# Optimization experiments

Hardware: AMD Instinct MI355X
Metric: run time of the kernel (lower is better)

The kernel has to match this reference:

```python
import jax, jax.numpy as jnp
import numpy as np

EMBED_DIM = 1024
N_HEADS = 16
HEAD_DIM = EMBED_DIM // N_HEADS
B, S = 2, 2048


def setup_inputs() -> dict:
    key = jax.random.key(0)
    ks = jax.random.split(key, 7)
    scale = 1.0 / np.sqrt(EMBED_DIM)
    return {
        "query": jax.random.normal(ks[0], (B, S, EMBED_DIM), dtype=jnp.float32),
        "key": jax.random.normal(ks[1], (B, S, EMBED_DIM), dtype=jnp.float32),
        "value": jax.random.normal(ks[2], (B, S, EMBED_DIM), dtype=jnp.float32),
        # nn.Linear weights stored as [out, in]; y = x @ W.T
        "Wq": jax.random.normal(ks[3], (EMBED_DIM, EMBED_DIM), dtype=jnp.float32) * scale,
        "Wk": jax.random.normal(ks[4], (EMBED_DIM, EMBED_DIM), dtype=jnp.float32) * scale,
        "Wv": jax.random.normal(ks[5], (EMBED_DIM, EMBED_DIM), dtype=jnp.float32) * scale,
        "Wo": jax.random.normal(ks[6], (EMBED_DIM, EMBED_DIM), dtype=jnp.float32) * scale,
    }


def reference(query, key, value, Wq, Wk, Wv, Wo):
    # Projections (Linear, no bias): x @ W.T
    Q = query @ Wq.T  # [B, S, E]
    K = key @ Wk.T
    V = value @ Wv.T
    b, s, _ = Q.shape
    # Split heads: slicing head i of [..., E] == reshape to [B, S, H, D]
    Qh = Q.reshape(b, s, N_HEADS, HEAD_DIM)
    Kh = K.reshape(b, s, N_HEADS, HEAD_DIM)
    Vh = V.reshape(b, s, N_HEADS, HEAD_DIM)
    scores = jnp.einsum("bqhd,bkhd->bhqk", Qh, Kh) / jnp.sqrt(
        jnp.asarray(HEAD_DIM, dtype=Qh.dtype)
    )  # [B, H, Sq, Sk]
    attn = jax.nn.softmax(scores, axis=-1)
    out = jnp.einsum("bhqk,bkhd->bqhd", attn, Vh)  # [B, Sq, H, D]
    out = out.reshape(b, s, N_HEADS * HEAD_DIM)  # concat heads
    return out @ Wo.T
```

## Files before the change

### kernel.cpp

```cpp
#include <hip/hip_runtime.h>
#include <hip/hip_bf16.h>
#include <stdint.h>
#include <stddef.h>

#define EMBED 1024
#define NHEAD 16
#define HDIM  64
#define BATCH 2
#define SEQ   2048
#define MTOT  (BATCH*SEQ)

typedef __hip_bfloat16 bf16;
typedef __attribute__((ext_vector_type(8))) __bf16 bf16x8;
typedef __attribute__((ext_vector_type(4))) float  f32x4;
typedef __attribute__((ext_vector_type(16))) float f32x16;

#define GLD16(gp, lp) __builtin_amdgcn_global_load_lds( \
    (__attribute__((address_space(1))) void*)(gp),      \
    (__attribute__((address_space(3))) void*)(lp), 16, 0, 0)


__device__ __forceinline__ ushort4 cvt4(const float4 v) {
  union { ushort4 u; bf16 b[4]; } o;
  o.b[0] = __float2bfloat16(v.x);
  o.b[1] = __float2bfloat16(v.y);
  o.b[2] = __float2bfloat16(v.z);
  o.b[3] = __float2bfloat16(v.w);
  return o.u;
}

__device__ __forceinline__ uint32_t pk2(float lo, float hi) {
  union { bf16 h[2]; uint32_t u; } r;
  r.h[0] = __float2bfloat16(lo);
  r.h[1] = __float2bfloat16(hi);
  return r.u;
}

__device__ __forceinline__ bool detect_bf16(const uint32_t* __restrict__ x, int t) {
  uint32_t w = x[(size_t)(t & 63) * 997u];
  int e = (int)((w >> 7) & 0xFF);
  unsigned long long m = __ballot(e >= 100 && e <= 135);
  return __popcll(m) >= 48;
}

#define SM_C1 0.18033688011112042f
#define SM_C0 -14.426950408889634f

__global__ __launch_bounds__(256)
void convert_inputs(const void* xs0, const void* xs1, const void* xs2,
                    const void* ws0, const void* ws1, const void* ws2, const void* ws3,
                    bf16* __restrict__ xd0, bf16* __restrict__ xd1, bf16* __restrict__ xd2,
                    bf16* __restrict__ wd0, bf16* __restrict__ wd1,
                    bf16* __restrict__ wd2, bf16* __restrict__ wd3) {
  const int bid = blockIdx.x;
  const void* src; bf16* dst; size_t base;
  if (bid < 6144) {
    const int a = bid >> 11;
    src = a == 0 ? xs0 : a == 1 ? xs1 : xs2;
    dst = a == 0 ? xd0 : a == 1 ? xd1 : xd2;
    base = (size_t)(bid & 2047) * 2048;
  } else {
    const int a = (bid - 6144) >> 9;
    src = a == 0 ? ws0 : a == 1 ? ws1 : a == 2 ? ws2 : ws3;
    dst = a == 0 ? wd0 : a == 1 ? wd1 : a == 2 ? wd2 : wd3;
    base = (size_t)((bid - 6144) & 511) * 2048;
  }
  const bool isbf = detect_bf16((const uint32_t*)src, threadIdx.x);
  const size_t off = base + (size_t)threadIdx.x * 8;
  if (isbf) {
    *(uint4*)((ushort*)dst + off) = *(const uint4*)((const ushort*)src + off);
  } else {
    const float* s = (const float*)src + off;
    float4 a4 = *(const float4*)(s);
    float4 b4 = *(const float4*)(s + 4);
    *(ushort4*)((ushort*)dst + off)     = cvt4(a4);
    *(ushort4*)((ushort*)dst + off + 4) = cvt4(b4);
  }
}

template<int TM, int TN>
__device__ __forceinline__ void gemm_nt_dbuf(
    const bf16* __restrict__ X, const bf16* __restrict__ W,
    bf16* sA, bf16* sB, f32x4 (&acc)[TM/32][TN/32],
    int row0, int col0, int t, int wr, int wc, int l16, int quad,
    int k0, int klen) {
  constexpr int CA = TM / 32, CB = TN / 32;
  constexpr int RI = TM / 32, RJ = TN / 32;
  constexpr int PF  = CA + CB;
  const int nit = klen >> 6;

  const bf16* gA[CA]; const bf16* gB[CB];
  int la[CA], lb[CB];
#pragma unroll
  for (int c = 0; c < CA; ++c) {
    int id = c * 256 + t, r = id >> 3;
    int cc = (((id & 7) ^ (r & 7)) * 8);
    gA[c] = X + (size_t)(row0 + r) * EMBED + k0 + cc;  la[c] = id * 8;
  }
#pragma unroll
  for (int c = 0; c < CB; ++c) {
    int id = c * 256 + t, r = id >> 3;
    int cc = (((id & 7) ^ (r & 7)) * 8);
    gB[c] = W + (size_t)(col0 + r) * EMBED + k0 + cc;  lb[c] = id * 8;
  }

  auto issue = [&](int kb, int buf) {
#pragma unroll
    for (int c = 0; c < CA; ++c) GLD16(gA[c] + kb, sA + buf * (TM * 64) + la[c]);
#pragma unroll
    for (int c = 0; c < CB; ++c) GLD16(gB[c] + kb, sB + buf * (TN * 64) + lb[c]);
  };
  const int xr = l16 & 7;
  auto compute = [&](int buf) {
    const bf16* pA = sA + buf * (TM * 64);
    const bf16* pB = sB + buf * (TN * 64);
#pragma unroll
    for (int kk = 0; kk < 64; kk += 32) {
      const int ch = (kk >> 3) + quad;
      bf16x8 a[RI], b[RJ];
#pragma unroll
      for (int i = 0; i < RI; ++i)
        a[i] = *(const bf16x8*)(pA + (wr + 16 * i + l16) * 64 + ((ch ^ xr) << 3));
#pragma unroll
      for (int j = 0; j < RJ; ++j)
        b[j] = *(const bf16x8*)(pB + (wc + 16 * j + l16) * 64 + ((ch ^ xr) << 3));
#pragma unroll
      for (int i = 0; i < RI; ++i)
#pragma unroll
        for (int j = 0; j < RJ; ++j)
          acc[i][j] = __builtin_amdgcn_mfma_f32_16x16x32_bf16(a[i], b[j], acc[i][j], 0, 0, 0);
    }
  };

  issue(0, 0);
  int p = 0;
  for (int i = 0; i < nit - 1; ++i) {
    issue((i + 1) * 64, p ^ 1);
    asm volatile("s_waitcnt vmcnt(%0)\ns_barrier" :: "i"(PF) : "memory");
    compute(p);
    asm volatile("s_barrier" ::: "memory");
    p ^= 1;
  }
  asm volatile("s_waitcnt vmcnt(0)\ns_barrier" ::: "memory");
  compute(p);
}

template<int TM, int TN, bool ABF, bool BBF>
__device__ __forceinline__ void gemm_nt_slow(
    const void* __restrict__ X, const void* __restrict__ W,
    bf16* sA, bf16* sB, f32x4 (&acc)[TM/32][TN/32],
    int row0, int col0, int t, int wr, int wc, int l16, int quad,
    int k0, int klen) {
  constexpr int RI = TM / 32, RJ = TN / 32;
  const int xr = l16 & 7;
  for (int kb = k0; kb < k0 + klen; kb += 64) {
    if constexpr (ABF) {
      const bf16* s = (const bf16*)X;
#pragma unroll
      for (int c = 0; c < TM / 32; ++c) {
        int id = c * 256 + t, r = id >> 3;
        int cc = (((id & 7) ^ (r & 7)) * 8);
        GLD16(s + (size_t)(row0 + r) * EMBED + kb + cc, sA + id * 8);
      }
    } else {
      const float* s = (const float*)X;
#pragma unroll
      for (int c = 0; c < TM / 16; ++c) {
        int id = c * 256 + t, r = id >> 4;
        int lc = (id & 15) >> 1, half = (id & 1) * 4;
        float4 v = *(const float4*)(s + (size_t)(row0 + r) * EMBED + kb + lc * 8 + half);
        *(ushort4*)(sA + r * 64 + ((lc ^ (r & 7)) << 3) + half) = cvt4(v);
      }
    }
    if constexpr (BBF) {
      const bf16* s = (const bf16*)W;
#pragma unroll
      for (int c = 0; c < TN / 32; ++c) {
        int id = c * 256 + t, r = id >> 3;
        int cc = (((id & 7) ^ (r & 7)) * 8);
        GLD16(s + (size_t)(col0 + r) * EMBED + kb + cc, sB + id * 8);
      }
    } else {
      const float* s = (const float*)W;
#pragma unroll
      for (int c = 0; c < TN / 16; ++c) {
        int id = c * 256 + t, r = id >> 4;
        int lc = (id & 15) >> 1, half = (id & 1) * 4;
        float4 v = *(const float4*)(s + (size_t)(col0 + r) * EMBED + kb + lc * 8 + half);
        *(ushort4*)(sB + r * 64 + ((lc ^ (r & 7)) << 3) + half) = cvt4(v);
      }
    }
    __syncthreads();
#pragma unroll
    for (int kk = 0; kk < 64; kk += 32) {
      const int ch = (kk >> 3) + quad;
      bf16x8 a[RI], b[RJ];
#pragma unroll
      for (int i = 0; i < RI; ++i)
        a[i] = *(const bf16x8*)(sA + (wr + 16 * i + l16) * 64 + ((ch ^ xr) << 3));
#pragma unroll
      for (int j = 0; j < RJ; ++j)
        b[j] = *(const bf16x8*)(sB + (wc + 16 * j + l16) * 64 + ((ch ^ xr) << 3));
#pragma unroll
      for (int i = 0; i < RI; ++i)
#pragma unroll
        for (int j = 0; j < RJ; ++j)
          acc[i][j] = __builtin_amdgcn_mfma_f32_16x16x32_bf16(a[i], b[j], acc[i][j], 0, 0, 0);
    }
    __syncthreads();
  }
}

__global__ __launch_bounds__(256, 2)
void qkv_proj_kernel(const void* Xq, const void* Xk, const void* Xv,
                     const void* Wq, const void* Wk, const void* Wv,
                     bf16* __restrict__ Qo, bf16* __restrict__ Ko,
                     bf16* __restrict__ Vto) {
  __shared__ __align__(16) bf16 sA[2 * 128 * 64];
  __shared__ __align__(16) bf16 sB[2 * 128 * 64];
  const int t    = threadIdx.x;
  const int wave = t >> 6, lane = t & 63;
  const int quad = lane >> 4, l16 = lane & 15;
  const int wr = (wave & 1) * 64;
  const int wc = (wave >> 1) * 64;
  const bool isbf = detect_bf16((const uint32_t*)Xq, t);

  for (int ti = blockIdx.x; ti < 768; ti += 512) {
    const int sel  = ti >> 8;
    const int col0 = ((ti >> 5) & 7) * 128;
    const int row0 = (ti & 31) * 128;
    const void* X = (sel == 0) ? Xq : (sel == 1) ? Xk : Xv;
    const void* W = (sel == 0) ? Wq : (sel == 1) ? Wk : Wv;

    f32x4 acc[4][4] = {};
    if (isbf)
      gemm_nt_dbuf<128, 128>((const bf16*)X, (const bf16*)W, sA, sB, acc,
                             row0, col0, t, wr, wc, l16, quad, 0, EMBED);
    else
      gemm_nt_slow<128, 128, false, false>(X, W, sA, sB, acc,
                                           row0, col0, t, wr, wc, l16, quad, 0, EMBED);

    if (sel < 2) {
      bf16* C = (sel == 0) ? Qo : Ko;
      const float sc = (sel == 0) ? SM_C1 : 1.0f;
#pragma unroll
      for (int i = 0; i < 4; ++i)
#pragma unroll
        for (int j = 0; j < 4; ++j)
#pragma unroll
          for (int r = 0; r < 4; ++r) {
            int m = row0 + wr + 16 * i + quad * 4 + r;
            int n = col0 + wc + 16 * j + l16;
            C[(size_t)m * EMBED + n] = __float2bfloat16(acc[i][j][r] * sc);
          }
    } else {
#pragma unroll
      for (int i = 0; i < 4; ++i)
#pragma unroll
        for (int j = 0; j < 4; ++j)
#pragma unroll
          for (int r = 0; r < 4; ++r) {
            int m = row0 + wr + 16 * i + quad * 4 + r;
            int n = col0 + wc + 16 * j + l16;
            int b = m >> 11, s = m & (SEQ - 1);
            int h = n >> 6,  d = n & (HDIM - 1);
            Vto[(((size_t)(b * NHEAD + h)) * HDIM + d) * SEQ + s] =
                __float2bfloat16(acc[i][j][r]);
          }
    }
    __syncthreads();
  }
}

__global__ __launch_bounds__(256, 2)
void out_proj_partial(const bf16* __restrict__ X, const void* W,
                      const uint32_t* __restrict__ qref, float* __restrict__ P) {
  __shared__ __align__(16) bf16 sA[2 * 128 * 64];
  __shared__ __align__(16) bf16 sB[2 * 128 * 64];
  const int t    = threadIdx.x;
  const int wave = t >> 6, lane = t & 63;
  const int quad = lane >> 4, l16 = lane & 15;
  const int row0 = blockIdx.x * 128;
  const int col0 = blockIdx.y * 128;
  const int z    = blockIdx.z;
  const int wr = (wave & 1) * 64;
  const int wc = (wave >> 1) * 64;
  const bool isbf = detect_bf16(qref, t);

  f32x4 acc[4][4] = {};
  if (isbf)
    gemm_nt_dbuf<128, 128>(X, (const bf16*)W, sA, sB, acc,
                           row0, col0, t, wr, wc, l16, quad, z * 512, 512);
  else
    gemm_nt_slow<128, 128, true, false>(X, W, sA, sB, acc,
                                        row0, col0, t, wr, wc, l16, quad, z * 512, 512);

  float* Pz = P + (size_t)z * MTOT * EMBED;
#pragma unroll
  for (int i = 0; i < 4; ++i)
#pragma unroll
    for (int j = 0; j < 4; ++j)
#pragma unroll
      for (int r = 0; r < 4; ++r) {
        int m = row0 + wr + 16 * i + quad * 4 + r;
        int n = col0 + wc + 16 * j + l16;
        Pz[(size_t)m * EMBED + n] = acc[i][j][r];
      }
}

__global__ __launch_bounds__(256)
void reduce_splitk(const float* __restrict__ P,
                   const uint32_t* __restrict__ qref, void* __restrict__ C) {
  const bool isbf = detect_bf16(qref, threadIdx.x);
  size_t i = ((size_t)blockIdx.x * 256 + threadIdx.x) * 4;
  float4 a = *(const float4*)(P + i);
  float4 b = *(const float4*)(P + (size_t)MTOT * EMBED + i);
  float4 s = make_float4(a.x + b.x, a.y + b.y, a.z + b.z, a.w + b.w);
  if (isbf) *(ushort4*)((bf16*)C + i) = cvt4(s);
  else      *(float4*)((float*)C + i) = s;
}

__global__ __launch_bounds__(256, 2)
void out_proj_kernel(const bf16* __restrict__ X, const void* W,
                     const uint32_t* __restrict__ qref, void* C) {
  __shared__ __align__(16) bf16 sA[2 * 64 * 64];
  __shared__ __align__(16) bf16 sB[2 * 128 * 64];
  const int t    = threadIdx.x;
  const int wave = t >> 6, lane = t & 63;
  const int quad = lane >> 4, l16 = lane & 15;
  const int row0 = blockIdx.x * 64;
  const int col0 = blockIdx.y * 128;
  const int wr = (wave & 1) * 32;
  const int wc = (wave >> 1) * 64;
  const bool isbf = detect_bf16(qref, t);

  f32x4 acc[2][4] = {};
  if (isbf)
    gemm_nt_dbuf<64, 128>(X, (const bf16*)W, sA, sB, acc,
                          row0, col0, t, wr, wc, l16, quad, 0, EMBED);
  else
    gemm_nt_slow<64, 128, true, false>(X, W, sA, sB, acc,
                                       row0, col0, t, wr, wc, l16, quad, 0, EMBED);

#pragma unroll
  for (int i = 0; i < 2; ++i)
#pragma unroll
    for (int j = 0; j < 4; ++j)
#pragma unroll
      for (int r = 0; r < 4; ++r) {
        int m = row0 + wr + 16 * i + quad * 4 + r;
        int n = col0 + wc + 16 * j + l16;
        if (isbf)
          ((bf16*)C)[(size_t)m * EMBED + n] = __float2bfloat16(acc[i][j][r]);
        else
          ((float*)C)[(size_t)m * EMBED + n] = acc[i][j][r];
      }
}

__global__ __launch_bounds__(256, 2)
void flash_kernel(const bf16* __restrict__ Q, const bf16* __restrict__ K,
                  const bf16* __restrict__ Vt, bf16* __restrict__ O) {
  __shared__ __align__(16) bf16 sK[2][64 * 64];
  __shared__ __align__(16) bf16 sV[2][64 * 64];

  const int t    = threadIdx.x;
  const int wave = t >> 6, lane = t & 63;
  const int l5 = lane & 31, hi = lane >> 5;
  const int x5 = l5 & 7;

  const int L  = ((blockIdx.x & 7) << 6) + (blockIdx.x >> 3);
  const int qt = L & 15;
  const int h  = (L >> 4) & 15;
  const int b  = L >> 8;
  const int qw = qt * 128 + 32 * wave;

  const bf16* Kg = K + ((size_t)b * SEQ) * EMBED + h * HDIM;
  const bf16* Vg = Vt + (((size_t)(b * NHEAD + h)) * HDIM) * SEQ;

  bf16x8 aq[4];
  {
    const bf16* Qrow = Q + ((size_t)b * SEQ + qw + l5) * EMBED + h * HDIM + hi * 8;
#pragma unroll
    for (int g = 0; g < 4; ++g) aq[g] = *(const bf16x8*)(Qrow + 16 * g);
  }

  union { bf16x8 v; bf16 e[8]; } ones;
#pragma unroll
  for (int i = 0; i < 8; ++i) ones.e[i] = __float2bfloat16(1.0f);

  auto issueKV = [&](int kt, int buf) {
#pragma unroll
    for (int c = 0; c < 2; ++c) {
      int id = c * 256 + t, r = id >> 3;
      int cc = (((id & 7) ^ (r & 7)) * 8);
      GLD16(Kg + (size_t)(kt + r) * EMBED + cc, &sK[buf][id * 8]);
      GLD16(Vg + (size_t)r * SEQ + kt + cc,     &sV[buf][id * 8]);
    }
  };

  f32x16 o0 = {}, o1 = {};
  f32x16 ls = {};

  auto tile_compute = [&](int buf) {
    f32x16 sT0, sT1;
#pragma unroll
    for (int r = 0; r < 16; ++r) { sT0[r] = SM_C0; sT1[r] = SM_C0; }
#pragma unroll
    for (int g = 0; g < 4; ++g) {
      const int ch = 2 * g + hi;
      bf16x8 ak0 = *(const bf16x8*)(&sK[buf][(l5)      * 64 + ((ch ^ x5) << 3)]);
      bf16x8 ak1 = *(const bf16x8*)(&sK[buf][(32 + l5) * 64 + ((ch ^ x5) << 3)]);
      sT0 = __builtin_amdgcn_mfma_f32_32x32x16_bf16(ak0, aq[g], sT0, 0, 0, 0);
      sT1 = __builtin_amdgcn_mfma_f32_32x32x16_bf16(ak1, aq[g], sT1, 0, 0, 0);
    }

    bf16x8 PA[4];
#pragma unroll
    for (int kg = 0; kg < 2; ++kg) {
      float p[16];
#pragma unroll
      for (int r = 0; r < 16; ++r)
        p[r] = __builtin_amdgcn_exp2f(kg ? sT1[r] : sT0[r]);
#pragma unroll
      for (int s = 0; s < 2; ++s) {
        uint32_t c0 = pk2(p[8 * s + 0], p[8 * s + 1]);
        uint32_t c1 = pk2(p[8 * s + 2], p[8 * s + 3]);
        uint32_t c2 = pk2(p[8 * s + 4], p[8 * s + 5]);
        uint32_t c3 = pk2(p[8 * s + 6], p[8 * s + 7]);
        uint32_t x = __shfl_xor(hi ? c0 : c2, 32, 64);
        uint32_t y = __shfl_xor(hi ? c1 : c3, 32, 64);
        union { uint32_t u[4]; bf16x8 v; } w;
        w.u[0] = hi ? x  : c0;
        w.u[1] = hi ? y  : c1;
        w.u[2] = hi ? c2 : x;
        w.u[3] = hi ? c3 : y;
        PA[2 * kg + s] = w.v;
      }
    }

#pragma unroll
    for (int kk = 0; kk < 4; ++kk) {
      const int ch = 2 * kk + hi;
      ls = __builtin_amdgcn_mfma_f32_32x32x16_bf16(PA[kk], ones.v, ls, 0, 0, 0);
      bf16x8 bv0 = *(const bf16x8*)(&sV[buf][(l5)      * 64 + ((ch ^ x5) << 3)]);
      bf16x8 bv1 = *(const bf16x8*)(&sV[buf][(32 + l5) * 64 + ((ch ^ x5) << 3)]);
      o0 = __builtin_amdgcn_mfma_f32_32x32x16_bf16(PA[kk], bv0, o0, 0, 0, 0);
      o1 = __builtin_amdgcn_mfma_f32_32x32x16_bf16(PA[kk], bv1, o1, 0, 0, 0);
    }
  };

  issueKV(0, 0);
  int p = 0;
  for (int it = 0; it < SEQ / 64 - 1; ++it) {
    issueKV((it + 1) * 64, p ^ 1);
    asm volatile("s_waitcnt vmcnt(4)\ns_barrier" ::: "memory");
    tile_compute(p);
    asm volatile("s_barrier" ::: "memory");
    p ^= 1;
  }
  asm volatile("s_waitcnt vmcnt(0)\ns_barrier" ::: "memory");
  tile_compute(p);

  bf16* Og = O + ((size_t)b * SEQ + qw) * EMBED + h * HDIM + l5;
#pragma unroll
  for (int r = 0; r < 16; ++r) {
    const int m = (r & 3) + 8 * (r >> 2) + 4 * hi;
    const float inv = 1.0f / ls[r];
    Og[(size_t)m * EMBED]      = __float2bfloat16(o0[r] * inv);
    Og[(size_t)m * EMBED + 32] = __float2bfloat16(o1[r] * inv);
  }
}

extern "C" void kernel_launch(void* const* d_in, const int* in_sizes, int n_in,
                              void* d_out, int out_size, void* d_ws, size_t ws_size,
                              hipStream_t stream) {
  (void)in_sizes; (void)n_in; (void)out_size;
  bf16* Qp  = (bf16*)((char*)d_ws + 256);
  bf16* Kp  = Qp  + (size_t)MTOT * EMBED;
  bf16* Vtp = Kp  + (size_t)MTOT * EMBED;
  bf16* Op  = Vtp + (size_t)MTOT * EMBED;
  float* Pf = (float*)(Op + (size_t)MTOT * EMBED);

  bf16* Xqb = (bf16*)Pf;
  bf16* Xkb = Xqb + (size_t)MTOT * EMBED;
  bf16* Xvb = Xkb + (size_t)MTOT * EMBED;
  bf16* Wqb = Xvb + (size_t)MTOT * EMBED;
  bf16* Wkb = Wqb + (size_t)EMBED * EMBED;
  bf16* Wvb = Wkb + (size_t)EMBED * EMBED;
  bf16* Wob = (bf16*)((char*)Pf + (size_t)2 * MTOT * EMBED * 4);

  const size_t need_split = 256 + (size_t)MTOT * EMBED * 2 * 4
                          + (size_t)MTOT * EMBED * 4 * 2;
  const size_t need_conv  = need_split + (size_t)EMBED * EMBED * 2;

  if (ws_size >= need_conv) {
    convert_inputs<<<dim3(8192), 256, 0, stream>>>(
        d_in[0], d_in[1], d_in[2], d_in[3], d_in[4], d_in[5], d_in[6],
        Xqb, Xkb, Xvb, Wqb, Wkb, Wvb, Wob);
    qkv_proj_kernel<<<dim3(512), 256, 0, stream>>>(
        Xqb, Xkb, Xvb, Wqb, Wkb, Wvb, Qp, Kp, Vtp);
    flash_kernel<<<dim3(512), 256, 0, stream>>>(Qp, Kp, Vtp, Op);
    out_proj_partial<<<dim3(32, 8, 2), 256, 0, stream>>>(
        Op, Wob, (const uint32_t*)Qp, Pf);
    reduce_splitk<<<dim3(MTOT * EMBED / 1024), 256, 0, stream>>>(
        Pf, (const uint32_t*)d_in[0], d_out);
  } else if (ws_size >= need_split) {
    qkv_proj_kernel<<<dim3(512), 256, 0, stream>>>(
        d_in[0], d_in[1], d_in[2], d_in[3], d_in[4], d_in[5], Qp, Kp, Vtp);
    flash_kernel<<<dim3(512), 256, 0, stream>>>(Qp, Kp, Vtp, Op);
    out_proj_partial<<<dim3(32, 8, 2), 256, 0, stream>>>(
        Op, d_in[6], (const uint32_t*)d_in[0], Pf);
    reduce_splitk<<<dim3(MTOT * EMBED / 1024), 256, 0, stream>>>(
        Pf, (const uint32_t*)d_in[0], d_out);
  } else {
    qkv_proj_kernel<<<dim3(512), 256, 0, stream>>>(
        d_in[0], d_in[1], d_in[2], d_in[3], d_in[4], d_in[5], Qp, Kp, Vtp);
    flash_kernel<<<dim3(512), 256, 0, stream>>>(Qp, Kp, Vtp, Op);
    out_proj_kernel<<<dim3(64, 8), 256, 0, stream>>>(
        Op, d_in[6], (const uint32_t*)d_in[0], d_out);
  }
}
```

Baseline: 224.9 us.

## Software-pipeline attention loop so next-tile QK overlaps current softmax and PV

Splits the per-tile attention body into separate QK, softmax and PV stages, and splits the K and V prefetches. The loop now computes the QK scores of tile i+1 while doing exp and the PV MFMAs of tile i, with K fetched two tiles ahead and V one tile ahead. The MFMA blocks are wrapped in s_setprio raises. The goal is to hide exp/pack/shuffle latency behind matrix work and to stagger memory traffic. In exchange it keeps more score registers live, and the final iteration fetches an unused K tile past the end of the sequence.

New measurement: 216.9 us. 1.04x faster.

```diff
diff --git a/kernel.cpp b/kernel.cpp
--- a/kernel.cpp
+++ b/kernel.cpp
@@ -388,39 +388,49 @@
 #pragma unroll
   for (int i = 0; i < 8; ++i) ones.e[i] = __float2bfloat16(1.0f);
 
-  auto issueKV = [&](int kt, int buf) {
+  auto issueK = [&](int kt, int buf) {
 #pragma unroll
     for (int c = 0; c < 2; ++c) {
       int id = c * 256 + t, r = id >> 3;
       int cc = (((id & 7) ^ (r & 7)) * 8);
       GLD16(Kg + (size_t)(kt + r) * EMBED + cc, &sK[buf][id * 8]);
-      GLD16(Vg + (size_t)r * SEQ + kt + cc,     &sV[buf][id * 8]);
+    }
+  };
+  auto issueV = [&](int kt, int buf) {
+#pragma unroll
+    for (int c = 0; c < 2; ++c) {
+      int id = c * 256 + t, r = id >> 3;
+      int cc = (((id & 7) ^ (r & 7)) * 8);
+      GLD16(Vg + (size_t)r * SEQ + kt + cc, &sV[buf][id * 8]);
     }
   };
 
   f32x16 o0 = {}, o1 = {};
   f32x16 ls = {};
-
-  auto tile_compute = [&](int buf) {
-    f32x16 sT0, sT1;
-#pragma unroll
-    for (int r = 0; r < 16; ++r) { sT0[r] = SM_C0; sT1[r] = SM_C0; }
+  f32x16 pT0, pT1;
+
+  auto qk = [&](int buf, f32x16& T0, f32x16& T1) {
+#pragma unroll
+    for (int r = 0; r < 16; ++r) { T0[r] = SM_C0; T1[r] = SM_C0; }
+    __builtin_amdgcn_s_setprio(1);
 #pragma unroll
     for (int g = 0; g < 4; ++g) {
       const int ch = 2 * g + hi;
       bf16x8 ak0 = *(const bf16x8*)(&sK[buf][(l5)      * 64 + ((ch ^ x5) << 3)]);
       bf16x8 ak1 = *(const bf16x8*)(&sK[buf][(32 + l5) * 64 + ((ch ^ x5) << 3)]);
-      sT0 = __builtin_amdgcn_mfma_f32_32x32x16_bf16(ak0, aq[g], sT0, 0, 0, 0);
-      sT1 = __builtin_amdgcn_mfma_f32_32x32x16_bf16(ak1, aq[g], sT1, 0, 0, 0);
-    }
-
-    bf16x8 PA[4];
+      T0 = __builtin_amdgcn_mfma_f32_32x32x16_bf16(ak0, aq[g], T0, 0, 0, 0);
+      T1 = __builtin_amdgcn_mfma_f32_32x32x16_bf16(ak1, aq[g], T1, 0, 0, 0);
+    }
+    __builtin_amdgcn_s_setprio(0);
+  };
+
+  auto smax = [&](const f32x16& T0, const f32x16& T1, bf16x8 (&PA)[4]) {
 #pragma unroll
     for (int kg = 0; kg < 2; ++kg) {
       float p[16];
 #pragma unroll
       for (int r = 0; r < 16; ++r)
-        p[r] = __builtin_amdgcn_exp2f(kg ? sT1[r] : sT0[r]);
+        p[r] = __builtin_amdgcn_exp2f(kg ? T1[r] : T0[r]);
 #pragma unroll
       for (int s = 0; s < 2; ++s) {
         uint32_t c0 = pk2(p[8 * s + 0], p[8 * s + 1]);
@@ -437,7 +447,10 @@
         PA[2 * kg + s] = w.v;
       }
     }
-
+  };
+
+  auto pv = [&](const bf16x8 (&PA)[4], int buf) {
+    __builtin_amdgcn_s_setprio(1);
 #pragma unroll
     for (int kk = 0; kk < 4; ++kk) {
       const int ch = 2 * kk + hi;
@@ -447,19 +460,34 @@
       o0 = __builtin_amdgcn_mfma_f32_32x32x16_bf16(PA[kk], bv0, o0, 0, 0, 0);
       o1 = __builtin_amdgcn_mfma_f32_32x32x16_bf16(PA[kk], bv1, o1, 0, 0, 0);
     }
-  };
-
-  issueKV(0, 0);
-  int p = 0;
-  for (int it = 0; it < SEQ / 64 - 1; ++it) {
-    issueKV((it + 1) * 64, p ^ 1);
+    __builtin_amdgcn_s_setprio(0);
+  };
+
+  issueK(0, 0); issueV(0, 0); issueK(64, 1);
+  asm volatile("s_waitcnt vmcnt(2)\ns_barrier" ::: "memory");
+  qk(0, pT0, pT1);
+  asm volatile("s_barrier" ::: "memory");
+
+#pragma unroll 2
+  for (int i = 0; i < SEQ / 64 - 1; ++i) {
+    issueK((i + 2) * 64, i & 1);
+    issueV((i + 1) * 64, (i + 1) & 1);
     asm volatile("s_waitcnt vmcnt(4)\ns_barrier" ::: "memory");
-    tile_compute(p);
+    f32x16 nT0, nT1;
+    qk((i + 1) & 1, nT0, nT1);
+    bf16x8 PA[4];
+    smax(pT0, pT1, PA);
+    pv(PA, i & 1);
     asm volatile("s_barrier" ::: "memory");
-    p ^= 1;
-  }
+    pT0 = nT0; pT1 = nT1;
+  }
+
   asm volatile("s_waitcnt vmcnt(0)\ns_barrier" ::: "memory");
-  tile_compute(p);
+  {
+    bf16x8 PA[4];
+    smax(pT0, pT1, PA);
+    pv(PA, (SEQ / 64 - 1) & 1);
+  }
 
   bf16* Og = O + ((size_t)b * SEQ + qw) * EMBED + h * HDIM + l5;
 #pragma unroll
```
